# Performance work log

Measured on AMD Instinct MI355X. Metric: run time of the kernel, lower is better.

## Reference

```python
import jax, jax.numpy as jnp
import numpy as np

B, S, D = 2, 2048, 2048
G, HPG = 4, 4            # n_groups, heads_per_group (n_heads=16)
DH = D // (G * HPG)      # head dim d_q = d_k = d_v = 128


def setup_inputs() -> dict:
    key = jax.random.key(0)
    ks = jax.random.split(key, 14)
    s = 1.0 / np.sqrt(D)
    inp = {
        "query": jax.random.normal(ks[0], (B, S, D), jnp.float32),
        "key":   jax.random.normal(ks[1], (B, S, D), jnp.float32),
        "value": jax.random.normal(ks[2], (B, S, D), jnp.float32),
        # per-group, per-head Q projections; per-group shared K, V
        "WQ": jax.random.normal(ks[3], (G, HPG, DH, D), jnp.float32) * s,
        "bQ": jax.random.normal(ks[4], (G, HPG, DH), jnp.float32) * 0.01,
        "WK": jax.random.normal(ks[5], (G, DH, D), jnp.float32) * s,
        "bK": jax.random.normal(ks[6], (G, DH), jnp.float32) * 0.01,
        "WV": jax.random.normal(ks[7], (G, DH, D), jnp.float32) * s,
        "bV": jax.random.normal(ks[8], (G, DH), jnp.float32) * 0.01,
        "WO": jax.random.normal(ks[9], (D, G * HPG * DH), jnp.float32) * s,
        "bO": jax.random.normal(ks[10], (D,), jnp.float32) * 0.01,
    }
    return inp


def reference(query, key, value, WQ, bQ, WK, bK, WV, bV, WO, bO):
    # q: [B, G, HPG, S, DH] — all per-head Q projections as one batched GEMM
    q = jnp.einsum('bsd,ghqd->bghsq', query, WQ) + bQ[None, :, :, None, :]
    # k, v: [B, G, S, DH] — one K/V per group (shared across heads in group)
    k = jnp.einsum('bsd,gkd->bgsk', key, WK) + bK[None, :, None, :]
    v = jnp.einsum('bsd,gvd->bgsv', value, WV) + bV[None, :, None, :]
    scale = 1.0 / jnp.sqrt(jnp.asarray(DH, q.dtype))
    # scores: [B, G, HPG, S_q, S_k]
    scores = jnp.einsum('bghsq,bgtq->bghst', q, k) * scale
    attn = jax.nn.softmax(scores, axis=-1)
    out = jnp.einsum('bghst,bgtv->bghsv', attn, v)   # [B, G, HPG, S, DH]
    # concat heads group-major, then transpose(1,2) + flatten like the torch code
    out = out.reshape(B, G * HPG, S, DH).transpose(0, 2, 1, 3).reshape(B, S, G * HPG * DH)
    return out @ WO.T + bO
```

## Files before the change

### kernel.cpp

```cpp
#include <hip/hip_runtime.h>
#include <cstdint>
#include <cstddef>


typedef __attribute__((ext_vector_type(8)))  __bf16 bf16x8;
typedef __attribute__((ext_vector_type(4)))  __bf16 bf16x4;
typedef __attribute__((ext_vector_type(4)))  float  f32x4;
typedef __attribute__((ext_vector_type(16))) float  f32x16;
typedef __attribute__((ext_vector_type(4)))  unsigned int u32x4;

#define GLD16(gp, lp) __builtin_amdgcn_global_load_lds(                         \
    (__attribute__((address_space(1))) void*)(size_t)(gp),                     \
    (__attribute__((address_space(3))) void*)(lp), 16, 0, 0)

#define PLSWAP(a, b) asm volatile("v_permlane32_swap_b32 %0, %1" : "+v"(a), "+v"(b))
#define EXP2F(x) __builtin_amdgcn_exp2f(x)

static __device__ __forceinline__ unsigned pack2bf(float a, float b) {
    unsigned short ua = __builtin_bit_cast(unsigned short, (__bf16)a);
    unsigned short ub = __builtin_bit_cast(unsigned short, (__bf16)b);
    return (unsigned)ua | ((unsigned)ub << 16);
}

struct F2BArgs {
    const float* src[7];
    __bf16* dst[7];
    long beg[8];
};
__global__ void f2b_multi(F2BArgs a) {
    const long total = a.beg[7];
    const long stride = (long)gridDim.x * blockDim.x;
    for (long i = (long)blockIdx.x * blockDim.x + threadIdx.x; i < total; i += stride) {
        int s = 0;
#pragma unroll
        for (int j = 1; j < 7; ++j) s += (i >= a.beg[j]);
        long off = i - a.beg[s];
        const float4* p = (const float4*)(a.src[s] + off * 8);
        float4 x = p[0], y = p[1];
        bf16x8 r;
        r[0] = (__bf16)x.x; r[1] = (__bf16)x.y; r[2] = (__bf16)x.z; r[3] = (__bf16)x.w;
        r[4] = (__bf16)y.x; r[5] = (__bf16)y.y; r[6] = (__bf16)y.z; r[7] = (__bf16)y.w;
        *(bf16x8*)(a.dst[s] + off * 8) = r;
    }
}

template <int OUTF32>
__global__ __launch_bounds__(512)
void gemm256(const __bf16* __restrict__ A, const __bf16* __restrict__ Bm,
             const float* __restrict__ bias, float* __restrict__ Cf,
             __bf16* __restrict__ Cb, int M, int N, int K, int nbx) {
    __shared__ __bf16 As[3][256 * 64];
    __shared__ __bf16 Bs[3][128 * 64];
    const int tid = threadIdx.x, lane = tid & 63, wid = tid >> 6;
    const int g = lane >> 4, c = lane & 15;
    const int wr = wid >> 1, wc = wid & 1;
    const int cpx = gridDim.x >> 3;
    const int swz = ((int)blockIdx.x & 7) * cpx + ((int)blockIdx.x >> 3);
    const int bx = swz % nbx, by = swz / nbx;
    const int m0 = by * 256, n0 = bx * 128;
    const int nkt = K >> 6;

    const f32x4 z = {0.f, 0.f, 0.f, 0.f};
    f32x4 acc[4][4];
#pragma unroll
    for (int i = 0; i < 4; ++i)
#pragma unroll
        for (int j = 0; j < 4; ++j) acc[i][j] = z;

    auto stageA = [&](int b, int kt, int h) {
        if (kt >= nkt) return;
        const __bf16* src = A + (size_t)m0 * K + (size_t)kt * 64;
#pragma unroll
        for (int i = 0; i < 2; ++i) {
            int ci = h * 1024 + i * 512 + tid;
            int row = ci >> 3, chg = (ci & 7) ^ (row & 7);
            GLD16(src + (size_t)row * K + chg * 8, &As[b][ci * 8]);
        }
    };
    auto stageB = [&](int b, int kt) {
        if (kt >= nkt) return;
        const __bf16* src = Bm + (size_t)n0 * K + (size_t)kt * 64;
#pragma unroll
        for (int i = 0; i < 2; ++i) {
            int ci = i * 512 + tid;
            int row = ci >> 3, chg = (ci & 7) ^ (row & 7);
            GLD16(src + (size_t)row * K + chg * 8, &Bs[b][ci * 8]);
        }
    };

    stageA(0, 0, 0); stageA(0, 0, 1); stageB(0, 0);
    stageA(1, 1, 0); stageA(1, 1, 1); stageB(1, 1);
    asm volatile("s_waitcnt vmcnt(6)" ::: "memory");
    __builtin_amdgcn_sched_barrier(0);
    __builtin_amdgcn_s_barrier();

    int bd = 0;
    for (int kt = 0; kt < nkt; ++kt) {
        const int bs = (bd >= 1) ? bd - 1 : 2;
        bf16x8 af[4], bfr[4];
#pragma unroll
        for (int ph = 0; ph < 2; ++ph) {
#pragma unroll
            for (int mi = 0; mi < 4; ++mi) {
                int row = wr * 64 + mi * 16 + c;
                int ch = (ph * 4 + g) ^ (c & 7);
                af[mi] = *(const bf16x8*)&As[bd][row * 64 + ch * 8];
            }
#pragma unroll
            for (int ni = 0; ni < 4; ++ni) {
                int row = wc * 64 + ni * 16 + c;
                int ch = (ph * 4 + g) ^ (c & 7);
                bfr[ni] = *(const bf16x8*)&Bs[bd][row * 64 + ch * 8];
            }
            if (ph == 0) {
                stageA(bs, kt + 2, 0);
            } else {
                stageA(bs, kt + 2, 1);
                stageB(bs, kt + 2);
            }
            __builtin_amdgcn_s_barrier();
            asm volatile("s_waitcnt lgkmcnt(0)" ::: "memory");
            __builtin_amdgcn_sched_barrier(0);
            __builtin_amdgcn_s_setprio(1);
#pragma unroll
            for (int mi = 0; mi < 4; ++mi)
#pragma unroll
                for (int ni = 0; ni < 4; ++ni)
                    acc[mi][ni] = __builtin_amdgcn_mfma_f32_16x16x32_bf16(
                        af[mi], bfr[ni], acc[mi][ni], 0, 0, 0);
            __builtin_amdgcn_s_setprio(0);
            if (ph == 1) {
                if (kt >= nkt - 2) asm volatile("s_waitcnt vmcnt(0)" ::: "memory");
                else               asm volatile("s_waitcnt vmcnt(6)" ::: "memory");
                __builtin_amdgcn_sched_barrier(0);
            }
            __builtin_amdgcn_s_barrier();
        }
        bd = (bd >= 2) ? 0 : bd + 1;
    }

#pragma unroll
    for (int mi = 0; mi < 4; ++mi) {
#pragma unroll
        for (int ni = 0; ni < 4; ++ni) {
            int col = n0 + wc * 64 + ni * 16 + c;
            float bvc = bias[col];
#pragma unroll
            for (int r = 0; r < 4; ++r) {
                int row = m0 + wr * 64 + mi * 16 + g * 4 + r;
                float v = acc[mi][ni][r] + bvc;
                if (OUTF32) Cf[(size_t)row * N + col] = v;
                else        Cb[(size_t)row * N + col] = (__bf16)v;
            }
        }
    }
}

static __device__ __forceinline__
void gemm_tile(const __bf16* __restrict__ A, const __bf16* __restrict__ Bm,
               const float* __restrict__ bias,
               __bf16* __restrict__ Cb, int N, int K, int m0, int n0, int biasrow,
               __bf16* As, __bf16* Bs) {
    const int tid = threadIdx.x;
    const int lane = tid & 63, wid = tid >> 6;
    const int g = lane >> 4, c = lane & 15;
    const int wr = wid >> 1, wc = wid & 1;

    const f32x4 z = {0.f, 0.f, 0.f, 0.f};
    f32x4 acc[4][4];
#pragma unroll
    for (int i = 0; i < 4; ++i)
#pragma unroll
        for (int j = 0; j < 4; ++j) acc[i][j] = z;

    const int nk = K >> 5;
#pragma unroll
    for (int i = 0; i < 2; ++i) {
        int ci = i * 256 + tid, row = ci >> 2, kc = (ci & 3) * 8;
        GLD16(A + (size_t)(m0 + row) * K + kc, As + ci * 8);
        GLD16(Bm + (size_t)(n0 + row) * K + kc, Bs + ci * 8);
    }
    __syncthreads();

    int cur = 0;
    for (int t = 0; t < nk; ++t) {
        if (t + 1 < nk) {
            int koff = (t + 1) * 32;
            int nb = (cur ^ 1) * 4096;
#pragma unroll
            for (int i = 0; i < 2; ++i) {
                int ci = i * 256 + tid, row = ci >> 2, kc = (ci & 3) * 8;
                GLD16(A + (size_t)(m0 + row) * K + koff + kc, As + nb + ci * 8);
                GLD16(Bm + (size_t)(n0 + row) * K + koff + kc, Bs + nb + ci * 8);
            }
        }
        int cb = cur * 4096;
        bf16x8 af[4], bfv[4];
#pragma unroll
        for (int im = 0; im < 4; ++im)
            af[im] = *(const bf16x8*)&As[cb + (wr * 64 + im * 16 + c) * 32 + g * 8];
#pragma unroll
        for (int in = 0; in < 4; ++in)
            bfv[in] = *(const bf16x8*)&Bs[cb + (wc * 64 + in * 16 + c) * 32 + g * 8];
        __builtin_amdgcn_s_setprio(1);
#pragma unroll
        for (int im = 0; im < 4; ++im)
#pragma unroll
            for (int in = 0; in < 4; ++in)
                acc[im][in] = __builtin_amdgcn_mfma_f32_16x16x32_bf16(
                    af[im], bfv[in], acc[im][in], 0, 0, 0);
        __builtin_amdgcn_s_setprio(0);
        __syncthreads();
        cur ^= 1;
    }

#pragma unroll
    for (int im = 0; im < 4; ++im) {
#pragma unroll
        for (int in = 0; in < 4; ++in) {
            int col = n0 + wc * 64 + in * 16 + c;
            float bvc = biasrow ? 0.f : bias[col];
#pragma unroll
            for (int r = 0; r < 4; ++r) {
                int row = m0 + wr * 64 + im * 16 + g * 4 + r;
                float v = acc[im][in][r] + (biasrow ? bias[row] : bvc);
                Cb[(size_t)row * N + col] = (__bf16)v;
            }
        }
    }
}

__global__ __launch_bounds__(256)
void gemm_kv(const __bf16* __restrict__ kb, const __bf16* __restrict__ wkb,
             const float* __restrict__ bK, __bf16* __restrict__ kp,
             const __bf16* __restrict__ wvb, const __bf16* __restrict__ vb,
             const float* __restrict__ bV, __bf16* __restrict__ vpT) {
    __shared__ __bf16 As[2 * 128 * 32];
    __shared__ __bf16 Bs[2 * 128 * 32];
    const int bid = blockIdx.x;
    const int swz = (bid & 7) * 32 + (bid >> 3);
    if (swz < 128) {
        int bx = swz & 31, by = swz >> 5;
        gemm_tile(kb, wkb, bK, kp, 512, 2048, bx * 128, by * 128, 0, As, Bs);
    } else {
        int s2 = swz - 128;
        int bx = s2 & 3, by = s2 >> 2;
        gemm_tile(wvb, vb, bV, vpT, 4096, 2048, bx * 128, by * 128, 1, As, Bs);
    }
}

__global__ __launch_bounds__(256)
void attn_kernel(const __bf16* __restrict__ Qw, const __bf16* __restrict__ Kw,
                 const __bf16* __restrict__ VTw, __bf16* __restrict__ Ow) {
    constexpr int S = 2048, DQ = 2048, DKV = 512, TOK = 4096;
    constexpr int nt = S / 64;
    const int bid = blockIdx.x;
    const int xcd = bid & 7, slot = bid >> 3;
    const int b = xcd >> 2, grp = xcd & 3;
    const int head = grp * 4 + (slot & 3);
    const int qblk = slot >> 2;
    const int t0 = slot & (nt - 1);
    const __bf16* Q   = Qw + (size_t)b * S * DQ + head * 128;
    const __bf16* Kp  = Kw + (size_t)b * S * DKV + grp * 128;
    const __bf16* VTp = VTw + (size_t)(grp * 128) * TOK + (size_t)b * S;
    __bf16* Op = Ow + (size_t)b * S * DQ + head * 128;

    __shared__ __bf16 Ks[2][64 * 128];
    __shared__ __bf16 Vs[2][128 * 64];

    const int tid = threadIdx.x, wid = tid >> 6, lane = tid & 63;
    const int ql = lane & 31, hi = lane >> 5;
    const int qrow = qblk * 128 + wid * 32 + ql;

    bf16x8 qf[8];
#pragma unroll
    for (int ks = 0; ks < 8; ++ks)
        qf[ks] = *(const bf16x8*)(Q + (size_t)qrow * DQ + ks * 16 + hi * 8);

    f32x16 o[4];
#pragma unroll
    for (int d = 0; d < 4; ++d)
#pragma unroll
        for (int r = 0; r < 16; ++r) o[d][r] = 0.f;
    float mprev = -1e30f, lsum = 0.f;
    constexpr float kexp = 0.08838834764831845f * 1.4426950408889634f;
    constexpr float THR = 8.0f / kexp;

    auto stage = [&](int buf, int t) {
#pragma unroll
        for (int i = 0; i < 4; ++i) {
            int ci = i * 256 + tid;
            int key = ci >> 4, ccl = ci & 15, ccg = ccl ^ (key & 15);
            GLD16(Kp + (size_t)(t * 64 + key) * DKV + ccg * 8, &Ks[buf][ci * 8]);
        }
#pragma unroll
        for (int i = 0; i < 4; ++i) {
            int ci = i * 256 + tid;
            int dh = ci >> 3, cl = ci & 7, cg = cl ^ ((dh ^ (dh >> 3)) & 7);
            GLD16(VTp + (size_t)dh * TOK + t * 64 + cg * 8, &Vs[buf][ci * 8]);
        }
    };

    stage(0, t0);
    __syncthreads();

    int cur = 0;
    for (int i = 0; i < nt; ++i) {
        if (i + 1 < nt) stage(cur ^ 1, (t0 + i + 1) & (nt - 1));

        f32x16 sc[2];
        __builtin_amdgcn_s_setprio(1);
#pragma unroll
        for (int kt = 0; kt < 2; ++kt) {
#pragma unroll
            for (int r = 0; r < 16; ++r) sc[kt][r] = 0.f;
#pragma unroll
            for (int ks = 0; ks < 8; ++ks) {
                int key = kt * 32 + ql;
                int chl = (ks * 2 + hi) ^ (key & 15);
                bf16x8 kf = *(const bf16x8*)&Ks[cur][key * 128 + chl * 8];
                sc[kt] = __builtin_amdgcn_mfma_f32_32x32x16_bf16(kf, qf[ks], sc[kt], 0, 0, 0);
            }
        }
        __builtin_amdgcn_s_setprio(0);

        float mo = sc[0][0];
#pragma unroll
        for (int r = 1; r < 16; ++r) mo = fmaxf(mo, sc[0][r]);
#pragma unroll
        for (int r = 0; r < 16; ++r) mo = fmaxf(mo, sc[1][r]);
        mo = fmaxf(mo, __shfl_xor(mo, 32, 64));
        if (!__all(mo - mprev <= THR)) {
            float mn = fmaxf(mprev, mo);
            float ef = EXP2F((mprev - mn) * kexp);
            lsum *= ef;
#pragma unroll
            for (int d = 0; d < 4; ++d)
#pragma unroll
                for (int r = 0; r < 16; ++r) o[d][r] *= ef;
            mprev = mn;
        }
        float mnk = mprev * kexp;
        float rs = 0.f;
#pragma unroll
        for (int kt = 0; kt < 2; ++kt)
#pragma unroll
            for (int r = 0; r < 16; ++r) {
                float p = EXP2F(__builtin_fmaf(sc[kt][r], kexp, -mnk));
                sc[kt][r] = p;
                rs += p;
            }
        rs += __shfl_xor(rs, 32, 64);
        lsum += rs;

        unsigned pk[2][4][2];
#pragma unroll
        for (int kt = 0; kt < 2; ++kt)
#pragma unroll
            for (int rg = 0; rg < 4; ++rg) {
                pk[kt][rg][0] = pack2bf(sc[kt][rg * 4 + 0], sc[kt][rg * 4 + 1]);
                pk[kt][rg][1] = pack2bf(sc[kt][rg * 4 + 2], sc[kt][rg * 4 + 3]);
            }

        __builtin_amdgcn_s_setprio(1);
#pragma unroll
        for (int ks = 0; ks < 4; ++ks) {
            const int kt = ks >> 1, e = ks & 1;
            unsigned a0 = pk[kt][2 * e][0], b0 = pk[kt][2 * e + 1][0];
            unsigned a1 = pk[kt][2 * e][1], b1 = pk[kt][2 * e + 1][1];
            PLSWAP(a0, b0);
            PLSWAP(a1, b1);
            u32x4 fw = {a0, a1, b0, b1};
            bf16x8 pf = __builtin_bit_cast(bf16x8, fw);
#pragma unroll
            for (int dht = 0; dht < 4; ++dht) {
                int dh = dht * 32 + ql;
                int chl = (ks * 2 + hi) ^ ((dh ^ (dh >> 3)) & 7);
                bf16x8 vf = *(const bf16x8*)&Vs[cur][dh * 64 + chl * 8];
                o[dht] = __builtin_amdgcn_mfma_f32_32x32x16_bf16(vf, pf, o[dht], 0, 0, 0);
            }
        }
        __builtin_amdgcn_s_setprio(0);
        __syncthreads();
        cur ^= 1;
    }

    float inv = 1.0f / lsum;
#pragma unroll
    for (int dht = 0; dht < 4; ++dht)
#pragma unroll
        for (int rg = 0; rg < 4; ++rg) {
            bf16x4 wv;
#pragma unroll
            for (int j = 0; j < 4; ++j) wv[j] = (__bf16)(o[dht][rg * 4 + j] * inv);
            int dh0 = dht * 32 + rg * 8 + hi * 4;
            *(bf16x4*)(Op + (size_t)qrow * DQ + dh0) = wv;
        }
}

extern "C" void kernel_launch(void* const* d_in, const int* in_sizes, int n_in,
                              void* d_out, int out_size, void* d_ws, size_t ws_size,
                              hipStream_t stream) {
    (void)in_sizes; (void)n_in; (void)out_size; (void)ws_size;
    const float* query = (const float*)d_in[0];
    const float* key   = (const float*)d_in[1];
    const float* value = (const float*)d_in[2];
    const float* WQ = (const float*)d_in[3];
    const float* bQ = (const float*)d_in[4];
    const float* WK = (const float*)d_in[5];
    const float* bK = (const float*)d_in[6];
    const float* WV = (const float*)d_in[7];
    const float* bV = (const float*)d_in[8];
    const float* WO = (const float*)d_in[9];
    const float* bO = (const float*)d_in[10];
    float* out = (float*)d_out;

    __bf16* w = (__bf16*)d_ws;
    __bf16* qb  = w; w += (size_t)4096 * 2048;
    __bf16* kb  = w; w += (size_t)4096 * 2048;
    __bf16* vb  = w; w += (size_t)4096 * 2048;
    __bf16* wqb = w; w += (size_t)2048 * 2048;
    __bf16* wkb = w; w += (size_t)512 * 2048;
    __bf16* wvb = w; w += (size_t)512 * 2048;
    __bf16* wob = w; w += (size_t)2048 * 2048;
    __bf16* qp  = w; w += (size_t)4096 * 2048;
    __bf16* kp  = w; w += (size_t)4096 * 512;
    __bf16* vpT = w; w += (size_t)512 * 4096;
    __bf16* ao  = w; w += (size_t)4096 * 2048;

    F2BArgs fa;
    fa.src[0] = query; fa.dst[0] = qb;
    fa.src[1] = key;   fa.dst[1] = kb;
    fa.src[2] = value; fa.dst[2] = vb;
    fa.src[3] = WQ;    fa.dst[3] = wqb;
    fa.src[4] = WK;    fa.dst[4] = wkb;
    fa.src[5] = WV;    fa.dst[5] = wvb;
    fa.src[6] = WO;    fa.dst[6] = wob;
    const long n8s[7] = {1048576, 1048576, 1048576, 524288, 131072, 131072, 524288};
    long acc = 0;
    for (int i = 0; i < 7; ++i) { fa.beg[i] = acc; acc += n8s[i]; }
    fa.beg[7] = acc;
    f2b_multi<<<2048, 256, 0, stream>>>(fa);

    gemm256<0><<<256, 512, 0, stream>>>(qb, wqb, bQ, nullptr, qp, 4096, 2048, 2048, 16);
    gemm_kv<<<256, 256, 0, stream>>>(kb, wkb, bK, kp, wvb, vb, bV, vpT);

    attn_kernel<<<512, 256, 0, stream>>>(qp, kp, vpT, ao);

    gemm256<1><<<256, 512, 0, stream>>>(ao, wob, bO, out, nullptr, 4096, 2048, 2048, 16);
}
```

Before: 271.3 us.

## Triple-buffer attention K/V tiles with 32-key blocks and partial vmcnt waits

Shrinks the attention key tile from 64 to 32 keys and moves from double to triple buffering in LDS, prefetching two tiles ahead. The full __syncthreads is replaced by an explicit s_waitcnt vmcnt(4) plus s_barrier, so the next tile's loads can stay in flight across the barrier. The aim is to hide global load latency better. In exchange there are twice as many loop iterations and barriers, shorter MFMA bursts per iteration, and a new V swizzle pattern.

```diff
diff --git a/kernel.cpp b/kernel.cpp
--- a/kernel.cpp
+++ b/kernel.cpp
@@ -253,7 +253,7 @@
 void attn_kernel(const __bf16* __restrict__ Qw, const __bf16* __restrict__ Kw,
                  const __bf16* __restrict__ VTw, __bf16* __restrict__ Ow) {
     constexpr int S = 2048, DQ = 2048, DKV = 512, TOK = 4096;
-    constexpr int nt = S / 64;
+    constexpr int nt = S / 32;
     const int bid = blockIdx.x;
     const int xcd = bid & 7, slot = bid >> 3;
     const int b = xcd >> 2, grp = xcd & 3;
@@ -265,8 +265,8 @@
     const __bf16* VTp = VTw + (size_t)(grp * 128) * TOK + (size_t)b * S;
     __bf16* Op = Ow + (size_t)b * S * DQ + head * 128;
 
-    __shared__ __bf16 Ks[2][64 * 128];
-    __shared__ __bf16 Vs[2][128 * 64];
+    __shared__ __bf16 Ks[3][32 * 128];
+    __shared__ __bf16 Vs[3][128 * 32];
 
     const int tid = threadIdx.x, wid = tid >> 6, lane = tid & 63;
     const int ql = lane & 31, hi = lane >> 5;
@@ -288,47 +288,44 @@
 
     auto stage = [&](int buf, int t) {
 #pragma unroll
-        for (int i = 0; i < 4; ++i) {
+        for (int i = 0; i < 2; ++i) {
             int ci = i * 256 + tid;
             int key = ci >> 4, ccl = ci & 15, ccg = ccl ^ (key & 15);
-            GLD16(Kp + (size_t)(t * 64 + key) * DKV + ccg * 8, &Ks[buf][ci * 8]);
-        }
-#pragma unroll
-        for (int i = 0; i < 4; ++i) {
+            GLD16(Kp + (size_t)(t * 32 + key) * DKV + ccg * 8, &Ks[buf][ci * 8]);
+        }
+#pragma unroll
+        for (int i = 0; i < 2; ++i) {
             int ci = i * 256 + tid;
-            int dh = ci >> 3, cl = ci & 7, cg = cl ^ ((dh ^ (dh >> 3)) & 7);
-            GLD16(VTp + (size_t)dh * TOK + t * 64 + cg * 8, &Vs[buf][ci * 8]);
+            int dh = ci >> 2, cl = ci & 3, cg = cl ^ ((dh >> 1) & 3);
+            GLD16(VTp + (size_t)dh * TOK + t * 32 + cg * 8, &Vs[buf][ci * 8]);
         }
     };
 
     stage(0, t0);
-    __syncthreads();
-
-    int cur = 0;
+    stage(1, (t0 + 1) & (nt - 1));
+    asm volatile("s_waitcnt vmcnt(4)" ::: "memory");
+    asm volatile("s_barrier" ::: "memory");
+
+    int bc = 0;
     for (int i = 0; i < nt; ++i) {
-        if (i + 1 < nt) stage(cur ^ 1, (t0 + i + 1) & (nt - 1));
-
-        f32x16 sc[2];
+        const int bs = (bc >= 1) ? bc - 1 : 2;
+        if (i + 2 < nt) stage(bs, (t0 + i + 2) & (nt - 1));
+
+        f32x16 sc;
+#pragma unroll
+        for (int r = 0; r < 16; ++r) sc[r] = 0.f;
         __builtin_amdgcn_s_setprio(1);
 #pragma unroll
-        for (int kt = 0; kt < 2; ++kt) {
-#pragma unroll
-            for (int r = 0; r < 16; ++r) sc[kt][r] = 0.f;
-#pragma unroll
-            for (int ks = 0; ks < 8; ++ks) {
-                int key = kt * 32 + ql;
-                int chl = (ks * 2 + hi) ^ (key & 15);
-                bf16x8 kf = *(const bf16x8*)&Ks[cur][key * 128 + chl * 8];
-                sc[kt] = __builtin_amdgcn_mfma_f32_32x32x16_bf16(kf, qf[ks], sc[kt], 0, 0, 0);
-            }
+        for (int ks = 0; ks < 8; ++ks) {
+            int chl = (ks * 2 + hi) ^ (ql & 15);
+            bf16x8 kf = *(const bf16x8*)&Ks[bc][ql * 128 + chl * 8];
+            sc = __builtin_amdgcn_mfma_f32_32x32x16_bf16(kf, qf[ks], sc, 0, 0, 0);
         }
         __builtin_amdgcn_s_setprio(0);
 
-        float mo = sc[0][0];
-#pragma unroll
-        for (int r = 1; r < 16; ++r) mo = fmaxf(mo, sc[0][r]);
-#pragma unroll
-        for (int r = 0; r < 16; ++r) mo = fmaxf(mo, sc[1][r]);
+        float mo = sc[0];
+#pragma unroll
+        for (int r = 1; r < 16; ++r) mo = fmaxf(mo, sc[r]);
         mo = fmaxf(mo, __shfl_xor(mo, 32, 64));
         if (!__all(mo - mprev <= THR)) {
             float mn = fmaxf(mprev, mo);
@@ -343,31 +340,26 @@
         float mnk = mprev * kexp;
         float rs = 0.f;
 #pragma unroll
-        for (int kt = 0; kt < 2; ++kt)
-#pragma unroll
-            for (int r = 0; r < 16; ++r) {
-                float p = EXP2F(__builtin_fmaf(sc[kt][r], kexp, -mnk));
-                sc[kt][r] = p;
-                rs += p;
-            }
+        for (int r = 0; r < 16; ++r) {
+            float p = EXP2F(__builtin_fmaf(sc[r], kexp, -mnk));
+            sc[r] = p;
+            rs += p;
+        }
         rs += __shfl_xor(rs, 32, 64);
         lsum += rs;
 
-        unsigned pk[2][4][2];
-#pragma unroll
-        for (int kt = 0; kt < 2; ++kt)
-#pragma unroll
-            for (int rg = 0; rg < 4; ++rg) {
-                pk[kt][rg][0] = pack2bf(sc[kt][rg * 4 + 0], sc[kt][rg * 4 + 1]);
-                pk[kt][rg][1] = pack2bf(sc[kt][rg * 4 + 2], sc[kt][rg * 4 + 3]);
-            }
+        unsigned pk[4][2];
+#pragma unroll
+        for (int rg = 0; rg < 4; ++rg) {
+            pk[rg][0] = pack2bf(sc[rg * 4 + 0], sc[rg * 4 + 1]);
+            pk[rg][1] = pack2bf(sc[rg * 4 + 2], sc[rg * 4 + 3]);
+        }
 
         __builtin_amdgcn_s_setprio(1);
 #pragma unroll
-        for (int ks = 0; ks < 4; ++ks) {
-            const int kt = ks >> 1, e = ks & 1;
-            unsigned a0 = pk[kt][2 * e][0], b0 = pk[kt][2 * e + 1][0];
-            unsigned a1 = pk[kt][2 * e][1], b1 = pk[kt][2 * e + 1][1];
+        for (int e = 0; e < 2; ++e) {
+            unsigned a0 = pk[2 * e][0], b0 = pk[2 * e + 1][0];
+            unsigned a1 = pk[2 * e][1], b1 = pk[2 * e + 1][1];
             PLSWAP(a0, b0);
             PLSWAP(a1, b1);
             u32x4 fw = {a0, a1, b0, b1};
@@ -375,14 +367,17 @@
 #pragma unroll
             for (int dht = 0; dht < 4; ++dht) {
                 int dh = dht * 32 + ql;
-                int chl = (ks * 2 + hi) ^ ((dh ^ (dh >> 3)) & 7);
-                bf16x8 vf = *(const bf16x8*)&Vs[cur][dh * 64 + chl * 8];
+                int chl = (e * 2 + hi) ^ ((dh >> 1) & 3);
+                bf16x8 vf = *(const bf16x8*)&Vs[bc][dh * 32 + chl * 8];
                 o[dht] = __builtin_amdgcn_mfma_f32_32x32x16_bf16(vf, pf, o[dht], 0, 0, 0);
             }
         }
         __builtin_amdgcn_s_setprio(0);
-        __syncthreads();
-        cur ^= 1;
+
+        if (i + 2 < nt) asm volatile("s_waitcnt vmcnt(4)" ::: "memory");
+        else            asm volatile("s_waitcnt vmcnt(0)" ::: "memory");
+        asm volatile("s_barrier" ::: "memory");
+        bc = (bc >= 2) ? 0 : bc + 1;
     }
 
     float inv = 1.0f / lsum;
```

New measurement: 262.1 us. -3.4%, faster.
